# Optimization experiments

Hardware: AMD Instinct MI355X
Metric: run time of the kernel (lower is better)

Reference implementation:

```python
import jax, jax.numpy as jnp
import numpy as np

NUM_CLASSES = 20
LAMBDA_COORD = 5.0
BATCH_SIZE = 512
ANCHORS = [[1.3221, 1.73145], [3.19275, 4.00944], [5.05587, 8.09892],
           [9.47112, 4.84053], [11.2364, 10.0071]]


def setup_inputs() -> dict:
    key = jax.random.key(0)
    k1, k2 = jax.random.split(key)
    prediction = jax.random.normal(k1, (512, 125, 13, 13), dtype=jnp.float32)
    # target: conf in [0,1), xy in [0,1), wh positive -> uniform is a valid fill
    target = jax.random.uniform(k2, (512, 13, 13, 125), dtype=jnp.float32)
    anchors = jnp.asarray(ANCHORS, dtype=jnp.float32)
    return {"prediction": prediction, "target": target, "anchors": anchors}


def _pairwise_iou(a, b):
    """a, b: [B, HW, A, 4] center-format (x, y, w, h).
    Returns pairwise IoU [B, HW, A, A] between a-anchors and b-boxes."""
    a = a[..., :, None, :]  # [B,HW,A,1,4]
    b = b[..., None, :, :]  # [B,HW,1,A,4]
    ax1, ay1 = a[..., 0] - a[..., 2] * 0.5, a[..., 1] - a[..., 3] * 0.5
    ax2, ay2 = a[..., 0] + a[..., 2] * 0.5, a[..., 1] + a[..., 3] * 0.5
    bx1, by1 = b[..., 0] - b[..., 2] * 0.5, b[..., 1] - b[..., 3] * 0.5
    bx2, by2 = b[..., 0] + b[..., 2] * 0.5, b[..., 1] + b[..., 3] * 0.5
    iw = jnp.clip(jnp.minimum(ax2, bx2) - jnp.maximum(ax1, bx1), 0.0)
    ih = jnp.clip(jnp.minimum(ay2, by2) - jnp.maximum(ay1, by1), 0.0)
    inter = iw * ih
    area_a = (ax2 - ax1) * (ay2 - ay1)
    area_b = (bx2 - bx1) * (by2 - by1)
    return inter / (area_a + area_b - inter + 1e-10)


def reference(prediction, target, anchors):
    bsize, _, h, w = prediction.shape
    A = anchors.shape[0]
    C = 5 + NUM_CLASSES
    out = jnp.transpose(prediction, (0, 2, 3, 1)).reshape(bsize, h * w * A, C)
    tgt = target.reshape(bsize, h * w * A, C)

    # decode predictions
    pred_xy = jax.nn.sigmoid(out[..., 21:23])
    pred_wh = jnp.exp(out[..., 23:25])
    pred_box = jnp.concatenate([pred_xy, pred_wh], axis=-1).reshape(bsize, h * w, A, 4)

    gt_box = jnp.concatenate([tgt[..., 21:23], tgt[..., 23:25]], axis=-1)
    gt_box = gt_box.reshape(bsize, h * w, A, 4)
    gt_conf = tgt[..., 20].reshape(bsize, h * w, A, 1)

    # anchor boxes: predicted centers with prior (anchor) width/height
    anc_wh = jnp.broadcast_to(anchors[None, None], (bsize, h * w, A, 2))
    anc_box = jnp.concatenate([pred_box[..., :2], anc_wh], axis=-1)

    iou = _pairwise_iou(anc_box, gt_box)            # [B, HW, A, A]
    anchor_idx = jnp.argmax(iou, axis=-1)           # [B, HW, A]

    # torch fancy-index write mask[:, :, anchor_idx, :] = gt_conf[:, :, anchor_idx, :]
    # assigns gt_conf at every anchor slot whose index appears anywhere in anchor_idx;
    # uncovered slots stay zero.
    covered = jnp.zeros((A,), dtype=bool).at[anchor_idx.reshape(-1)].set(True)
    mask = jnp.where(covered[None, None, :, None], gt_conf, 0.0)

    diff = pred_box * mask - gt_box * mask
    box_loss = (LAMBDA_COORD / BATCH_SIZE) * jnp.sum(diff * diff)
    return box_loss
```

## Files before the change

### kernel.cpp

```cpp
#include <hip/hip_runtime.h>
#include <math.h>

#define NB 512
#define HW 169
#define NA 5
#define NCH 125
#define BLOCK 256
#define NPAIRS (NB * HW * NA)
#define NBLOCKS (NPAIRS / BLOCK)
#define REC 8

__global__ __launch_bounds__(BLOCK, 4) void yolo_loss_main(
    const float* __restrict__ P,
    const float* __restrict__ T,
    const float* __restrict__ ANC,
    float* __restrict__ brec)
{
    int t = threadIdx.x;
    int pid  = blockIdx.x * BLOCK + t;
    int cell = pid / NA;
    int a    = pid - cell * NA;
    int b  = cell / HW;
    int hw = cell - b * HW;

    const float* Tc = T + (size_t)cell * NCH;
    const float* Pb = P + (size_t)b * NCH * HW + hw;

    float g[20];
#pragma unroll
    for (int j = 0; j < NA; ++j) {
        g[j * 4 + 0] = Tc[j * 25 + 21];
        g[j * 4 + 1] = Tc[j * 25 + 22];
        g[j * 4 + 2] = Tc[j * 25 + 23];
        g[j * 4 + 3] = Tc[j * 25 + 24];
    }
    float conf = Tc[a * 25 + 20];
    float rx = Pb[(a * 25 + 21) * HW];
    float ry = Pb[(a * 25 + 22) * HW];
    float rw = Pb[(a * 25 + 23) * HW];
    float rh = Pb[(a * 25 + 24) * HW];
    float aw = ANC[2 * a], ah = ANC[2 * a + 1];

    float px = 1.0f / (1.0f + expf(-rx));
    float py = 1.0f / (1.0f + expf(-ry));
    float pw = expf(rw);
    float ph = expf(rh);

    float ax1 = px - aw * 0.5f, ax2 = px + aw * 0.5f;
    float ay1 = py - ah * 0.5f, ay2 = py + ah * 0.5f;
    float area_a = (ax2 - ax1) * (ay2 - ay1);
    float best = -1.0f; int bestj = 0;
    float gxa = 0.f, gya = 0.f, gwa = 0.f, gha = 0.f;
#pragma unroll
    for (int j = 0; j < NA; ++j) {
        float bx = g[j * 4 + 0], by = g[j * 4 + 1];
        float bw = g[j * 4 + 2], bh = g[j * 4 + 3];
        float bx1 = bx - bw * 0.5f, bx2 = bx + bw * 0.5f;
        float by1 = by - bh * 0.5f, by2 = by + bh * 0.5f;
        float iw = fmaxf(fminf(ax2, bx2) - fmaxf(ax1, bx1), 0.0f);
        float ih = fmaxf(fminf(ay2, by2) - fmaxf(ay1, by1), 0.0f);
        float inter = iw * ih;
        float area_b = (bx2 - bx1) * (by2 - by1);
        float iou = inter / (area_a + area_b - inter + 1e-10f);
        if (iou > best) { best = iou; bestj = j; }
        if (j == a) { gxa = bx; gya = by; gwa = bw; gha = bh; }
    }
    int cmask = 1 << bestj;

    float dx = px - gxa, dy = py - gya, dw = pw - gwa, dh = ph - gha;
    float contrib = conf * conf * (dx * dx + dy * dy + dw * dw + dh * dh);

    __shared__ float sred[4][NA];
    __shared__ int smask[4];
    int lane = t & 63, wid = t >> 6;

#pragma unroll
    for (int i = 0; i < NA; ++i) {
        float v = (a == i) ? contrib : 0.0f;
        for (int off = 32; off; off >>= 1) v += __shfl_down(v, off, 64);
        if (lane == 0) sred[wid][i] = v;
    }
    for (int off = 32; off; off >>= 1) cmask |= __shfl_down(cmask, off, 64);
    if (lane == 0) smask[wid] = cmask;
    __syncthreads();

    if (t == 0) {
        int m = smask[0] | smask[1] | smask[2] | smask[3];
        float4* r4 = (float4*)(brec + blockIdx.x * REC);
        r4[0] = make_float4(sred[0][0] + sred[1][0] + sred[2][0] + sred[3][0],
                            sred[0][1] + sred[1][1] + sred[2][1] + sred[3][1],
                            sred[0][2] + sred[1][2] + sred[2][2] + sred[3][2],
                            sred[0][3] + sred[1][3] + sred[2][3] + sred[3][3]);
        r4[1] = make_float4(sred[0][4] + sred[1][4] + sred[2][4] + sred[3][4],
                            __int_as_float(m), 0.0f, 0.0f);
    }
}

__global__ __launch_bounds__(256) void yolo_loss_final(
    const float* __restrict__ brec, float* __restrict__ out)
{
    __shared__ double sredd[4][NA];
    __shared__ int smaskd[4];
    int t = threadIdx.x, lane = t & 63, wid = t >> 6;
    const float4* r4 = (const float4*)brec;

    double s[NA] = {0, 0, 0, 0, 0};
    int m = 0;
    for (int e = t; e < NBLOCKS; e += 256) {
        float4 lo = r4[e * 2];
        float4 hi = r4[e * 2 + 1];
        s[0] += (double)lo.x; s[1] += (double)lo.y;
        s[2] += (double)lo.z; s[3] += (double)lo.w;
        s[4] += (double)hi.x;
        m |= __float_as_int(hi.y);
    }
#pragma unroll
    for (int i = 0; i < NA; ++i)
        for (int off = 32; off; off >>= 1) s[i] += __shfl_down(s[i], off, 64);
    for (int off = 32; off; off >>= 1) m |= __shfl_down(m, off, 64);
    if (lane == 0) {
#pragma unroll
        for (int i = 0; i < NA; ++i) sredd[wid][i] = s[i];
        smaskd[wid] = m;
    }
    __syncthreads();

    if (t == 0) {
        int mm = smaskd[0] | smaskd[1] | smaskd[2] | smaskd[3];
        double tot = 0.0;
#pragma unroll
        for (int i = 0; i < NA; ++i)
            if ((mm >> i) & 1)
                tot += sredd[0][i] + sredd[1][i] + sredd[2][i] + sredd[3][i];
        out[0] = (float)((5.0 / 512.0) * tot);
    }
}

extern "C" void kernel_launch(void* const* d_in, const int* in_sizes, int n_in,
                              void* d_out, int out_size, void* d_ws, size_t ws_size,
                              hipStream_t stream) {
    const float* P   = (const float*)d_in[0];
    const float* T   = (const float*)d_in[1];
    const float* ANC = (const float*)d_in[2];
    float* out = (float*)d_out;

    float* brec = (float*)d_ws;

    yolo_loss_main<<<NBLOCKS, BLOCK, 0, stream>>>(P, T, ANC, brec);
    yolo_loss_final<<<1, 256, 0, stream>>>(brec, out);
}
```

Before: 20.21 us.

## Stage per-block target slab into LDS with coalesced float4 loads

Each block now handles 64 cells (320 threads) and cooperatively copies the contiguous target slab for those cells into shared memory using float4 loads, then reads gt boxes and confidence from LDS. This replaces strided per-thread global reads that were duplicated across the five anchor threads of a cell. It costs 32 KB of LDS per block, which limits occupancy, and loads all channels rather than only the needed ones. The reduction is extended to five wavefronts.

```diff
diff --git a/kernel.cpp b/kernel.cpp
--- a/kernel.cpp
+++ b/kernel.cpp
@@ -5,41 +5,59 @@
 #define HW 169
 #define NA 5
 #define NCH 125
-#define BLOCK 256
-#define NPAIRS (NB * HW * NA)
-#define NBLOCKS (NPAIRS / BLOCK)
+#define CELLS 64
+#define BLOCK (CELLS * NA)
+#define NBLOCKS ((NB * HW) / CELLS)
+#define SLAB_F4 ((CELLS * NCH) / 4)
 #define REC 8
 
-__global__ __launch_bounds__(BLOCK, 4) void yolo_loss_main(
+__global__ __launch_bounds__(BLOCK) void yolo_loss_main(
     const float* __restrict__ P,
     const float* __restrict__ T,
     const float* __restrict__ ANC,
     float* __restrict__ brec)
 {
+    __shared__ float sT[CELLS * NCH];
     int t = threadIdx.x;
-    int pid  = blockIdx.x * BLOCK + t;
-    int cell = pid / NA;
-    int a    = pid - cell * NA;
+
+    {
+        const float4* T4 = (const float4*)T + (size_t)blockIdx.x * SLAB_F4;
+        float4* s4 = (float4*)sT;
+#pragma unroll
+        for (int k = 0; k < 7; ++k) {
+            int li = t + k * BLOCK;
+            if (li < SLAB_F4) s4[li] = T4[li];
+        }
+    }
+
+    int cl = t / NA;
+    int a  = t - cl * NA;
+    int cell = blockIdx.x * CELLS + cl;
     int b  = cell / HW;
     int hw = cell - b * HW;
+    const float* Pb = P + (size_t)b * (NCH * HW) + hw + (a * 25 + 21) * HW;
+    float rx = Pb[0];
+    float ry = Pb[HW];
+    float rw = Pb[2 * HW];
+    float rh = Pb[3 * HW];
+    float aw = ANC[2 * a], ah = ANC[2 * a + 1];
 
-    const float* Tc = T + (size_t)cell * NCH;
-    const float* Pb = P + (size_t)b * NCH * HW + hw;
+    __syncthreads();
 
+    const float* sc = sT + cl * NCH;
     float g[20];
 #pragma unroll
     for (int j = 0; j < NA; ++j) {
-        g[j * 4 + 0] = Tc[j * 25 + 21];
-        g[j * 4 + 1] = Tc[j * 25 + 22];
-        g[j * 4 + 2] = Tc[j * 25 + 23];
-        g[j * 4 + 3] = Tc[j * 25 + 24];
+        g[j * 4 + 0] = sc[j * 25 + 21];
+        g[j * 4 + 1] = sc[j * 25 + 22];
+        g[j * 4 + 2] = sc[j * 25 + 23];
+        g[j * 4 + 3] = sc[j * 25 + 24];
     }
-    float conf = Tc[a * 25 + 20];
-    float rx = Pb[(a * 25 + 21) * HW];
-    float ry = Pb[(a * 25 + 22) * HW];
-    float rw = Pb[(a * 25 + 23) * HW];
-    float rh = Pb[(a * 25 + 24) * HW];
-    float aw = ANC[2 * a], ah = ANC[2 * a + 1];
+    float conf = sc[a * 25 + 20];
+    float gxa  = sc[a * 25 + 21];
+    float gya  = sc[a * 25 + 22];
+    float gwa  = sc[a * 25 + 23];
+    float gha  = sc[a * 25 + 24];
 
     float px = 1.0f / (1.0f + expf(-rx));
     float py = 1.0f / (1.0f + expf(-ry));
@@ -50,7 +68,6 @@
     float ay1 = py - ah * 0.5f, ay2 = py + ah * 0.5f;
     float area_a = (ax2 - ax1) * (ay2 - ay1);
     float best = -1.0f; int bestj = 0;
-    float gxa = 0.f, gya = 0.f, gwa = 0.f, gha = 0.f;
 #pragma unroll
     for (int j = 0; j < NA; ++j) {
         float bx = g[j * 4 + 0], by = g[j * 4 + 1];
@@ -63,15 +80,14 @@
         float area_b = (bx2 - bx1) * (by2 - by1);
         float iou = inter / (area_a + area_b - inter + 1e-10f);
         if (iou > best) { best = iou; bestj = j; }
-        if (j == a) { gxa = bx; gya = by; gwa = bw; gha = bh; }
     }
     int cmask = 1 << bestj;
 
     float dx = px - gxa, dy = py - gya, dw = pw - gwa, dh = ph - gha;
     float contrib = conf * conf * (dx * dx + dy * dy + dw * dw + dh * dh);
 
-    __shared__ float sred[4][NA];
-    __shared__ int smask[4];
+    __shared__ float sred[5][NA];
+    __shared__ int smask[5];
     int lane = t & 63, wid = t >> 6;
 
 #pragma unroll
@@ -85,14 +101,14 @@
     __syncthreads();
 
     if (t == 0) {
-        int m = smask[0] | smask[1] | smask[2] | smask[3];
+        int m = smask[0] | smask[1] | smask[2] | smask[3] | smask[4];
+        float s[NA];
+#pragma unroll
+        for (int i = 0; i < NA; ++i)
+            s[i] = sred[0][i] + sred[1][i] + sred[2][i] + sred[3][i] + sred[4][i];
         float4* r4 = (float4*)(brec + blockIdx.x * REC);
-        r4[0] = make_float4(sred[0][0] + sred[1][0] + sred[2][0] + sred[3][0],
-                            sred[0][1] + sred[1][1] + sred[2][1] + sred[3][1],
-                            sred[0][2] + sred[1][2] + sred[2][2] + sred[3][2],
-                            sred[0][3] + sred[1][3] + sred[2][3] + sred[3][3]);
-        r4[1] = make_float4(sred[0][4] + sred[1][4] + sred[2][4] + sred[3][4],
-                            __int_as_float(m), 0.0f, 0.0f);
+        r4[0] = make_float4(s[0], s[1], s[2], s[3]);
+        r4[1] = make_float4(s[4], __int_as_float(m), 0.0f, 0.0f);
     }
 }
 
```

Result: slower. 22.93 us (+13.4%).
